# Kernel tuning notes

Hardware: AMD Instinct MI355X
Metric: run time of the kernel (lower is better)

The kernel has to match this reference:

```python
import jax, jax.numpy as jnp
import numpy as np

N_NODES = 100000
IN_CH, HID_CH, OUT_CH = 128, 256, 128
N_EDGES = 1600000
N_LABEL = 200000


def setup_inputs() -> dict:
    key = jax.random.key(0)
    ks = jax.random.split(key, 9)
    x = jax.random.normal(ks[0], (N_NODES, IN_CH), dtype=jnp.float32)
    edge_index = jax.random.randint(ks[1], (2, N_EDGES), 0, N_NODES, dtype=jnp.int64)
    edge_label_index = jax.random.randint(ks[2], (2, N_LABEL), 0, N_NODES, dtype=jnp.int64)
    def glorot(k, fan_in, fan_out):
        s = jnp.sqrt(2.0 / (fan_in + fan_out))
        return jax.random.normal(k, (fan_in, fan_out), dtype=jnp.float32) * s
    # SAGEConv params: lin_l (aggregated neighbors, with bias), lin_r (root, no bias)
    Wl1 = glorot(ks[3], IN_CH, HID_CH)
    bl1 = jnp.zeros((HID_CH,), dtype=jnp.float32)
    Wr1 = glorot(ks[4], IN_CH, HID_CH)
    Wl2 = glorot(ks[5], HID_CH, OUT_CH)
    bl2 = jnp.zeros((OUT_CH,), dtype=jnp.float32)
    Wr2 = glorot(ks[6], HID_CH, OUT_CH)
    return {"x": x, "edge_index": edge_index, "edge_label_index": edge_label_index,
            "Wl1": Wl1, "bl1": bl1, "Wr1": Wr1, "Wl2": Wl2, "bl2": bl2, "Wr2": Wr2}


def _sage_conv(x, src, dst, Wl, bl, Wr):
    # mean aggregation of source-node messages onto destination nodes
    n = x.shape[0]
    agg = jax.ops.segment_sum(x[src], dst, num_segments=n)          # [N, d]
    deg = jax.ops.segment_sum(jnp.ones_like(dst, dtype=x.dtype), dst, num_segments=n)
    agg = agg / jnp.maximum(deg, 1.0)[:, None]
    return agg @ Wl + bl + x @ Wr


def reference(x, edge_index, edge_label_index, Wl1, bl1, Wr1, Wl2, bl2, Wr2):
    src, dst = edge_index[0], edge_index[1]
    h = jax.nn.relu(_sage_conv(x, src, dst, Wl1, bl1, Wr1))
    z = _sage_conv(h, src, dst, Wl2, bl2, Wr2)                      # [N, out]
    lsrc, ldst = edge_label_index[0], edge_label_index[1]
    return jnp.sum(z[lsrc] * z[ldst], axis=-1)                      # [E_label]
```

## Files before the change

kernel.cpp:

```cpp
#include <hip/hip_runtime.h>

#define N_NODES 100000
#define N_EDGES 1600000
#define N_LABEL 200000
#define C_IN 128
#define C_HID 256
#define C_OUT 128

#define BCHUNK 64
#define NBUCK ((N_NODES + BCHUNK - 1) / BCHUNK)
#define NBF 64
#define EPB (N_EDGES / NBF)
#define FLEN (NBUCK * NBF)
#define ESTORE 2048
#define CAST_NB ((N_NODES * C_IN) / (256 * 8))
#define SBLK ((FLEN + 1023) / 1024)

typedef __attribute__((ext_vector_type(8))) short bf16x8;
typedef __attribute__((ext_vector_type(4))) float f32x4;

__device__ __forceinline__ ushort f2bf(float f) {
  uint u = __float_as_uint(f);
  return (ushort)((u + 0x7fffu + ((u >> 16) & 1u)) >> 16);
}

__device__ __forceinline__ uint pack2(float lo, float hi) {
  return (uint)f2bf(lo) | ((uint)f2bf(hi) << 16);
}

__device__ __forceinline__ float bfl(uint u) { return __uint_as_float(u << 16); }
__device__ __forceinline__ float bfh(uint u) {
  return __uint_as_float(u & 0xffff0000u);
}

__device__ __forceinline__ void async_copy16(const void* g, void* lds) {
  __builtin_amdgcn_global_load_lds((const __attribute__((address_space(1))) void*)g,
                                   (__attribute__((address_space(3))) void*)lds,
                                   16, 0, 0);
}

__global__ __launch_bounds__(256) void prep_kernel(const int* __restrict__ dst,
                                                   int* __restrict__ cnt,
                                                   const float* __restrict__ Wl1,
                                                   const float* __restrict__ Wr1,
                                                   const float* __restrict__ Wl2,
                                                   const float* __restrict__ Wr2,
                                                   ushort* __restrict__ WT1,
                                                   ushort* __restrict__ WT2,
                                                   const float* __restrict__ x,
                                                   ushort* __restrict__ xb) {
  __shared__ int lcnt[NBUCK];
  const int blk = blockIdx.x;
  const int t = threadIdx.x;
  if (blk < NBF) {
    const int base = blk * EPB;
    for (int b = t; b < NBUCK; b += 256) lcnt[b] = 0;
    __syncthreads();
    for (int i = t; i < EPB; i += 256) {
      atomicAdd(&lcnt[dst[base + i] >> 6], 1);
    }
    __syncthreads();
    for (int b = t; b < NBUCK; b += 256) cnt[b * NBF + blk] = lcnt[b];
  } else if (blk < NBF + 256) {
    const int n = blk - NBF;
    const int k = t;
    const float v1 = (k < 128) ? Wl1[k * 256 + n] : Wr1[(k - 128) * 256 + n];
    WT1[n * 256 + k] = f2bf(v1);
    const float v2 = (n < 128) ? Wl2[k * 128 + n] : Wr2[k * 128 + (n - 128)];
    WT2[n * 256 + k] = f2bf(v2);
  } else {
    const size_t i = ((size_t)(blk - NBF - 256) * 256 + t) * 8;
    const float4 a = *(const float4*)&x[i];
    const float4 b = *(const float4*)&x[i + 4];
    uint4 o;
    o.x = pack2(a.x, a.y);
    o.y = pack2(a.z, a.w);
    o.z = pack2(b.x, b.y);
    o.w = pack2(b.z, b.w);
    *(uint4*)&xb[i] = o;
  }
}

__global__ __launch_bounds__(256) void scan_sums(const int* __restrict__ a,
                                                 int* __restrict__ bsum) {
  __shared__ int red[256];
  const int t = threadIdx.x;
  const int idx = blockIdx.x * 1024 + t * 4;
  int s = 0;
  if (idx + 3 < FLEN) {
    const int4 v = *(const int4*)&a[idx];
    s = v.x + v.y + v.z + v.w;
  } else {
    for (int j = 0; j < 4 && idx + j < FLEN; ++j) s += a[idx + j];
  }
  red[t] = s;
  __syncthreads();
  for (int off = 128; off > 0; off >>= 1) {
    if (t < off) red[t] += red[t + off];
    __syncthreads();
  }
  if (t == 0) bsum[blockIdx.x] = red[0];
}

__global__ __launch_bounds__(256) void scan_apply(int* __restrict__ a,
                                                  const int* __restrict__ bsum) {
  __shared__ int sh[256];
  __shared__ int bsc[128];
  const int t = threadIdx.x;
  if (t < 128) bsc[t] = (t < SBLK) ? bsum[t] : 0;
  __syncthreads();
  for (int off = 1; off < 128; off <<= 1) {
    int v = 0;
    if (t < 128 && t >= off) v = bsc[t - off];
    __syncthreads();
    if (t < 128 && t >= off) bsc[t] += v;
    __syncthreads();
  }
  const int bbase = (blockIdx.x == 0) ? 0 : bsc[blockIdx.x - 1];
  if (blockIdx.x == SBLK - 1 && t == 0) a[FLEN] = bsc[SBLK - 1];

  const int idx = blockIdx.x * 1024 + t * 4;
  int4 v = make_int4(0, 0, 0, 0);
  const bool full = (idx + 3 < FLEN);
  if (full) {
    v = *(const int4*)&a[idx];
  } else {
    if (idx + 0 < FLEN) v.x = a[idx + 0];
    if (idx + 1 < FLEN) v.y = a[idx + 1];
    if (idx + 2 < FLEN) v.z = a[idx + 2];
    if (idx + 3 < FLEN) v.w = a[idx + 3];
  }
  sh[t] = v.x + v.y + v.z + v.w;
  __syncthreads();
  for (int off = 1; off < 256; off <<= 1) {
    int u = 0;
    if (t >= off) u = sh[t - off];
    __syncthreads();
    if (t >= off) sh[t] += u;
    __syncthreads();
  }
  const int base = bbase + ((t == 0) ? 0 : sh[t - 1]);
  int4 e;
  e.x = base;
  e.y = base + v.x;
  e.z = base + v.x + v.y;
  e.w = base + v.x + v.y + v.z;
  if (full) {
    *(int4*)&a[idx] = e;
  } else {
    if (idx + 0 < FLEN) a[idx + 0] = e.x;
    if (idx + 1 < FLEN) a[idx + 1] = e.y;
    if (idx + 2 < FLEN) a[idx + 2] = e.z;
    if (idx + 3 < FLEN) a[idx + 3] = e.w;
  }
}

__global__ __launch_bounds__(256) void bucket_fill(const int* __restrict__ src,
                                                   const int* __restrict__ dst,
                                                   const int* __restrict__ cnt,
                                                   uint* __restrict__ tmp) {
  __shared__ int lcur[NBUCK];
  const int t = threadIdx.x;
  const int base = blockIdx.x * EPB;
  for (int b = t; b < NBUCK; b += 256) lcur[b] = cnt[b * NBF + blockIdx.x];
  __syncthreads();
  for (int i = t; i < EPB; i += 256) {
    const int d = dst[base + i];
    const int s = src[base + i];
    const int pos = atomicAdd(&lcur[d >> 6], 1);
    tmp[pos] = ((uint)s << 6) | (uint)(d & 63);
  }
}

__global__ __launch_bounds__(256) void csr_build(const int* __restrict__ cnt,
                                                 uint* __restrict__ tmp,
                                                 int* __restrict__ row_start) {
  __shared__ uint est[ESTORE];
  __shared__ uint eso[ESTORE];
  __shared__ int lcnt[BCHUNK];
  __shared__ int lcur[BCHUNK];
  const int b = blockIdx.x;
  const int t = threadIdx.x;
  const int s = cnt[b * NBF];
  const int e = cnt[(b + 1) * NBF];
  const int n = e - s;
  for (int j = t; j < n; j += 256) est[j] = tmp[s + j];
  if (t < BCHUNK) lcnt[t] = 0;
  __syncthreads();
  for (int j = t; j < n; j += 256) atomicAdd(&lcnt[est[j] & 63], 1);
  __syncthreads();
  for (int off = 1; off < BCHUNK; off <<= 1) {
    int v = 0;
    if (t >= off && t < BCHUNK) v = lcnt[t - off];
    __syncthreads();
    if (t >= off && t < BCHUNK) lcnt[t] += v;
    __syncthreads();
  }
  if (t < BCHUNK) {
    const int ex = (t == 0) ? 0 : lcnt[t - 1];
    lcur[t] = ex;
    const int node = b * BCHUNK + t;
    if (node < N_NODES) row_start[node] = s + ex;
  }
  if (b == NBUCK - 1 && t == 0) row_start[N_NODES] = e;
  __syncthreads();
  for (int j = t; j < n; j += 256) {
    const uint v = est[j];
    const int pos = atomicAdd(&lcur[v & 63], 1);
    eso[pos] = v >> 6;
  }
  __syncthreads();
  for (int j = t; j < n; j += 256) tmp[s + j] = eso[j];
}

template <int MODE>
__global__ __launch_bounds__(256) void gather_mean_b(const int* __restrict__ row_start,
                                                     const uint* __restrict__ csr_src,
                                                     const ushort* __restrict__ feat,
                                                     ushort* __restrict__ bout,
                                                     ushort* __restrict__ zb) {
  const int wid = blockIdx.x * 4 + (threadIdx.x >> 6);
  const int lane = threadIdx.x & 63;
  if (wid >= N_NODES) return;
  const int s = row_start[wid];
  const int e = row_start[wid + 1];
  const int slot = lane >> 4;
  const int c0 = (lane & 15) * 8;
  float acc[8] = {};
  int j = s + slot;
#define ACC8(r)                                   \
  acc[0] += bfl(r.x); acc[1] += bfh(r.x);         \
  acc[2] += bfl(r.y); acc[3] += bfh(r.y);         \
  acc[4] += bfl(r.z); acc[5] += bfh(r.z);         \
  acc[6] += bfl(r.w); acc[7] += bfh(r.w);
  for (; j + 12 < e; j += 16) {
    const uint s0 = csr_src[j];
    const uint s1 = csr_src[j + 4];
    const uint s2 = csr_src[j + 8];
    const uint s3 = csr_src[j + 12];
    const uint4 r0 = *(const uint4*)&feat[(size_t)s0 * 128 + c0];
    const uint4 r1 = *(const uint4*)&feat[(size_t)s1 * 128 + c0];
    const uint4 r2 = *(const uint4*)&feat[(size_t)s2 * 128 + c0];
    const uint4 r3 = *(const uint4*)&feat[(size_t)s3 * 128 + c0];
    ACC8(r0) ACC8(r1) ACC8(r2) ACC8(r3)
  }
  for (; j < e; j += 4) {
    const uint s0 = csr_src[j];
    const uint4 r0 = *(const uint4*)&feat[(size_t)s0 * 128 + c0];
    ACC8(r0)
  }
#undef ACC8
#pragma unroll
  for (int k = 0; k < 8; ++k) {
    acc[k] += __shfl_xor(acc[k], 16, 64);
    acc[k] += __shfl_xor(acc[k], 32, 64);
  }
  if (slot == 0) {
    const float rd = 1.0f / fmaxf((float)(e - s), 1.0f);
    if (MODE == 0) {
      uint4 o;
      o.x = pack2(acc[0] * rd, acc[1] * rd);
      o.y = pack2(acc[2] * rd, acc[3] * rd);
      o.z = pack2(acc[4] * rd, acc[5] * rd);
      o.w = pack2(acc[6] * rd, acc[7] * rd);
      *(uint4*)&bout[(size_t)wid * 128 + c0] = o;
    } else {
      uint4 zv = *(const uint4*)&zb[(size_t)wid * 128 + c0];
      uint4 o;
      o.x = pack2(bfl(zv.x) + acc[0] * rd, bfh(zv.x) + acc[1] * rd);
      o.y = pack2(bfl(zv.y) + acc[2] * rd, bfh(zv.y) + acc[3] * rd);
      o.z = pack2(bfl(zv.z) + acc[4] * rd, bfh(zv.z) + acc[5] * rd);
      o.w = pack2(bfl(zv.w) + acc[6] * rd, bfh(zv.w) + acc[7] * rd);
      *(uint4*)&zb[(size_t)wid * 128 + c0] = o;
    }
  }
}

__global__ __launch_bounds__(256) void gemm_fused(const ushort* __restrict__ aggb,
                                                  const ushort* __restrict__ xb,
                                                  const ushort* __restrict__ WT1,
                                                  const ushort* __restrict__ WT2,
                                                  const float* __restrict__ bl1,
                                                  const float* __restrict__ bl2,
                                                  ushort* __restrict__ p,
                                                  ushort* __restrict__ zb) {
  __shared__ ushort As[2048];
  __shared__ ushort Bs[8192];
  __shared__ ushort Ht[64 * 256];
  const int tid = threadIdx.x;
  const int w = tid >> 6;
  const int l = tid & 63;
  const int row0 = blockIdx.x * 64;
  const int wn = w * 64;
  const int fr = l & 15;
  const int kg16 = (l >> 4) * 16;
  const int cr = (l >> 4) * 4;
  const int cc = l & 15;

  const int arow = tid >> 2;
  const int akb = (tid & 3) * 16;
  const int akbs = akb ^ (((arow >> 1) & 3) << 4);
  int agr = row0 + arow;
  agr = (agr < N_NODES) ? agr : (N_NODES - 1);
  const int brow_l = l >> 2;
  const int bkb = (l & 3) * 16;

  {
    f32x4 acc[4][4] = {};
    for (int kc = 0; kc < 8; ++kc) {
      const ushort* Ab = (kc < 4) ? aggb : xb;
      __syncthreads();
      async_copy16((const char*)Ab + (size_t)agr * 256 + (kc & 3) * 64 + akbs,
                   (char*)As + w * 1024);
#pragma unroll
      for (int i_ = 0; i_ < 4; ++i_) {
        const int c_ = w * 4 + i_;
        const int n_ = c_ * 16 + brow_l;
        const int kbs_ = bkb ^ (((n_ >> 1) & 3) << 4);
        async_copy16((const char*)WT1 + (size_t)n_ * 512 + kc * 64 + kbs_,
                     (char*)Bs + c_ * 1024);
      }
      __syncthreads();
      bf16x8 af[4], bfr[4];
#pragma unroll
      for (int i = 0; i < 4; ++i) {
        const int ra = i * 16 + fr;
        const int ba = ra * 64 + (kg16 ^ (((ra >> 1) & 3) << 4));
        af[i] = *(const bf16x8*)((const char*)As + ba);
      }
#pragma unroll
      for (int j = 0; j < 4; ++j) {
        const int nb = wn + j * 16 + fr;
        const int bb = nb * 64 + (kg16 ^ (((nb >> 1) & 3) << 4));
        bfr[j] = *(const bf16x8*)((const char*)Bs + bb);
      }
#pragma unroll
      for (int i = 0; i < 4; ++i)
#pragma unroll
        for (int j = 0; j < 4; ++j)
          acc[i][j] = __builtin_amdgcn_mfma_f32_16x16x32_bf16(af[i], bfr[j],
                                                              acc[i][j], 0, 0, 0);
    }
#pragma unroll
    for (int i = 0; i < 4; ++i) {
#pragma unroll
      for (int j = 0; j < 4; ++j) {
        const int col = wn + j * 16 + cc;
        const float bv = bl1[col];
#pragma unroll
        for (int r = 0; r < 4; ++r) {
          const int row = i * 16 + cr + r;
          const float v = fmaxf(acc[i][j][r] + bv, 0.f);
          const int ba = (row * 512 + col * 2) ^ ((row & 7) << 4);
          *(ushort*)((char*)Ht + ba) = f2bf(v);
        }
      }
    }
  }
  __syncthreads();

  f32x4 acc2[4][4] = {};
#pragma unroll
  for (int kc = 0; kc < 8; ++kc) {
    bf16x8 af[4], bfr[4];
#pragma unroll
    for (int i = 0; i < 4; ++i) {
      const int row = i * 16 + fr;
      const int ba = (row * 512 + kc * 64 + kg16) ^ ((row & 7) << 4);
      af[i] = *(const bf16x8*)((const char*)Ht + ba);
    }
#pragma unroll
    for (int j = 0; j < 4; ++j) {
      const int n = wn + j * 16 + fr;
      bfr[j] = *(const bf16x8*)((const char*)WT2 + (size_t)n * 512 + kc * 64 +
                                kg16);
    }
#pragma unroll
    for (int i = 0; i < 4; ++i)
#pragma unroll
      for (int j = 0; j < 4; ++j)
        acc2[i][j] = __builtin_amdgcn_mfma_f32_16x16x32_bf16(af[i], bfr[j],
                                                             acc2[i][j], 0, 0, 0);
  }
#pragma unroll
  for (int i = 0; i < 4; ++i) {
#pragma unroll
    for (int j = 0; j < 4; ++j) {
      const int col = wn + j * 16 + cc;
      const int gcl = col & 127;
      const bool is_p = (col < 128);
      const float bv = is_p ? 0.f : bl2[gcl];
      ushort* dst = is_p ? p : zb;
#pragma unroll
      for (int r = 0; r < 4; ++r) {
        const int grow = row0 + i * 16 + cr + r;
        if (grow < N_NODES) {
          dst[(size_t)grow * 128 + gcl] = f2bf(acc2[i][j][r] + bv);
        }
      }
    }
  }
}

__global__ __launch_bounds__(256) void dot_kernel(const int* __restrict__ ls,
                                                  const int* __restrict__ ld,
                                                  const ushort* __restrict__ zb,
                                                  float* __restrict__ out) {
  long long tid = (long long)blockIdx.x * 256 + threadIdx.x;
  int e = (int)(tid >> 4);
  int lane = (int)(tid & 15);
  if (e >= N_LABEL) return;
  int a = ls[e], b = ld[e];
  const uint4 va = *(const uint4*)&zb[(size_t)a * 128 + lane * 8];
  const uint4 vb = *(const uint4*)&zb[(size_t)b * 128 + lane * 8];
  float s = bfl(va.x) * bfl(vb.x) + bfh(va.x) * bfh(vb.x) +
            bfl(va.y) * bfl(vb.y) + bfh(va.y) * bfh(vb.y) +
            bfl(va.z) * bfl(vb.z) + bfh(va.z) * bfh(vb.z) +
            bfl(va.w) * bfl(vb.w) + bfh(va.w) * bfh(vb.w);
  s += __shfl_xor(s, 1, 16);
  s += __shfl_xor(s, 2, 16);
  s += __shfl_xor(s, 4, 16);
  s += __shfl_xor(s, 8, 16);
  if (lane == 0) out[e] = s;
}

extern "C" void kernel_launch(void* const* d_in, const int* in_sizes, int n_in,
                              void* d_out, int out_size, void* d_ws, size_t ws_size,
                              hipStream_t stream) {
  const float* x = (const float*)d_in[0];
  const int* ei = (const int*)d_in[1];
  const int* eli = (const int*)d_in[2];
  const float* Wl1 = (const float*)d_in[3];
  const float* bl1 = (const float*)d_in[4];
  const float* Wr1 = (const float*)d_in[5];
  const float* Wl2 = (const float*)d_in[6];
  const float* bl2 = (const float*)d_in[7];
  const float* Wr2 = (const float*)d_in[8];
  float* out = (float*)d_out;

  const int* e_src = ei;
  const int* e_dst = ei + N_EDGES;
  const int* l_src = eli;
  const int* l_dst = eli + N_LABEL;

  char* ws = (char*)d_ws;
  ushort* xb = (ushort*)(ws + 0);
  ushort* aggb = (ushort*)(ws + 25600000);
  ushort* p = (ushort*)(ws + 102400000);
  ushort* zb = (ushort*)(ws + 128000000);
  ushort* WT1 = (ushort*)(ws + 179200000);
  ushort* WT2 = (ushort*)(ws + 179331072);
  uint* tmp = (uint*)(ws + 179462144);
  int* cnt = (int*)(ws + 185862144);
  int* bsum = (int*)(ws + 186270000);
  int* row_start = (int*)(ws + 186280000);

  prep_kernel<<<NBF + 256 + CAST_NB, 256, 0, stream>>>(
      e_dst, cnt, Wl1, Wr1, Wl2, Wr2, WT1, WT2, x, xb);
  scan_sums<<<SBLK, 256, 0, stream>>>(cnt, bsum);
  scan_apply<<<SBLK, 256, 0, stream>>>(cnt, bsum);
  bucket_fill<<<NBF, 256, 0, stream>>>(e_src, e_dst, cnt, tmp);
  csr_build<<<NBUCK, 256, 0, stream>>>(cnt, tmp, row_start);

  gather_mean_b<0><<<(N_NODES + 3) / 4, 256, 0, stream>>>(row_start, tmp, xb,
                                                          aggb, nullptr);
  gemm_fused<<<(N_NODES + 63) / 64, 256, 0, stream>>>(aggb, xb, WT1, WT2, bl1,
                                                      bl2, p, zb);
  gather_mean_b<1><<<(N_NODES + 3) / 4, 256, 0, stream>>>(row_start, tmp, p,
                                                          nullptr, zb);

  dot_kernel<<<(int)(((long long)N_LABEL * 16 + 255) / 256), 256, 0, stream>>>(
      l_src, l_dst, zb, out);
}
```

Baseline: 304.9 us.

## Stage full A tile once in shared memory and read first-layer weights from global

The fused GEMM kernel now loads the whole 64x512 concatenated [agg|x] row tile into one shared buffer up front, replacing the eight per-k-chunk A/B staging rounds and their barriers. First-layer weight fragments are read straight from global or cache, as the second layer already did. The same buffer is reused to hold the ReLU hidden activations after a barrier, which cuts shared memory per block and should allow higher occupancy. The cost is that every wave now issues uncoalesced global weight loads inside the MFMA loop.

```diff
diff --git a/kernel.cpp b/kernel.cpp
--- a/kernel.cpp
+++ b/kernel.cpp
@@ -284,9 +284,7 @@
                                                   const float* __restrict__ bl2,
                                                   ushort* __restrict__ p,
                                                   ushort* __restrict__ zb) {
-  __shared__ ushort As[2048];
-  __shared__ ushort Bs[8192];
-  __shared__ ushort Ht[64 * 256];
+  __shared__ ushort AH[64 * 256];
   const int tid = threadIdx.x;
   const int w = tid >> 6;
   const int l = tid & 63;
@@ -297,77 +295,71 @@
   const int cr = (l >> 4) * 4;
   const int cc = l & 15;
 
-  const int arow = tid >> 2;
-  const int akb = (tid & 3) * 16;
-  const int akbs = akb ^ (((arow >> 1) & 3) << 4);
-  int agr = row0 + arow;
-  agr = (agr < N_NODES) ? agr : (N_NODES - 1);
-  const int brow_l = l >> 2;
-  const int bkb = (l & 3) * 16;
-
-  {
-    f32x4 acc[4][4] = {};
-    for (int kc = 0; kc < 8; ++kc) {
-      const ushort* Ab = (kc < 4) ? aggb : xb;
-      __syncthreads();
-      async_copy16((const char*)Ab + (size_t)agr * 256 + (kc & 3) * 64 + akbs,
-                   (char*)As + w * 1024);
-#pragma unroll
-      for (int i_ = 0; i_ < 4; ++i_) {
-        const int c_ = w * 4 + i_;
-        const int n_ = c_ * 16 + brow_l;
-        const int kbs_ = bkb ^ (((n_ >> 1) & 3) << 4);
-        async_copy16((const char*)WT1 + (size_t)n_ * 512 + kc * 64 + kbs_,
-                     (char*)Bs + c_ * 1024);
-      }
-      __syncthreads();
-      bf16x8 af[4], bfr[4];
-#pragma unroll
-      for (int i = 0; i < 4; ++i) {
-        const int ra = i * 16 + fr;
-        const int ba = ra * 64 + (kg16 ^ (((ra >> 1) & 3) << 4));
-        af[i] = *(const bf16x8*)((const char*)As + ba);
-      }
-#pragma unroll
-      for (int j = 0; j < 4; ++j) {
-        const int nb = wn + j * 16 + fr;
-        const int bb = nb * 64 + (kg16 ^ (((nb >> 1) & 3) << 4));
-        bfr[j] = *(const bf16x8*)((const char*)Bs + bb);
-      }
-#pragma unroll
-      for (int i = 0; i < 4; ++i)
-#pragma unroll
-        for (int j = 0; j < 4; ++j)
-          acc[i][j] = __builtin_amdgcn_mfma_f32_16x16x32_bf16(af[i], bfr[j],
-                                                              acc[i][j], 0, 0, 0);
-    }
-#pragma unroll
-    for (int i = 0; i < 4; ++i) {
-#pragma unroll
-      for (int j = 0; j < 4; ++j) {
-        const int col = wn + j * 16 + cc;
-        const float bv = bl1[col];
-#pragma unroll
-        for (int r = 0; r < 4; ++r) {
-          const int row = i * 16 + cr + r;
-          const float v = fmaxf(acc[i][j][r] + bv, 0.f);
-          const int ba = (row * 512 + col * 2) ^ ((row & 7) << 4);
-          *(ushort*)((char*)Ht + ba) = f2bf(v);
-        }
-      }
-    }
-  }
-  __syncthreads();
-
-  f32x4 acc2[4][4] = {};
+#pragma unroll
+  for (int it = 0; it < 8; ++it) {
+    const int r = it * 8 + w * 2 + (l >> 5);
+    const int cb = (l & 31) * 16;
+    const int cbs = cb ^ ((r & 7) << 4);
+    int node = row0 + r;
+    node = (node < N_NODES) ? node : (N_NODES - 1);
+    const char* src = (cbs < 256)
+        ? (const char*)aggb + (size_t)node * 256 + cbs
+        : (const char*)xb + (size_t)node * 256 + (cbs - 256);
+    async_copy16(src, (char*)AH + it * 4096 + w * 1024);
+  }
+  __syncthreads();
+
+  f32x4 acc[4][4] = {};
 #pragma unroll
   for (int kc = 0; kc < 8; ++kc) {
     bf16x8 af[4], bfr[4];
 #pragma unroll
     for (int i = 0; i < 4; ++i) {
+      const int ra = i * 16 + fr;
+      const int ba = ra * 512 + ((kc * 64 + kg16) ^ ((ra & 7) << 4));
+      af[i] = *(const bf16x8*)((const char*)AH + ba);
+    }
+#pragma unroll
+    for (int j = 0; j < 4; ++j) {
+      const int n = wn + j * 16 + fr;
+      bfr[j] = *(const bf16x8*)((const char*)WT1 + (size_t)n * 512 + kc * 64 +
+                                kg16);
+    }
+#pragma unroll
+    for (int i = 0; i < 4; ++i)
+#pragma unroll
+      for (int j = 0; j < 4; ++j)
+        acc[i][j] = __builtin_amdgcn_mfma_f32_16x16x32_bf16(af[i], bfr[j],
+                                                            acc[i][j], 0, 0, 0);
+  }
+  __syncthreads();
+
+#pragma unroll
+  for (int i = 0; i < 4; ++i) {
+#pragma unroll
+    for (int j = 0; j < 4; ++j) {
+      const int col = wn + j * 16 + cc;
+      const float bv = bl1[col];
+#pragma unroll
+      for (int r = 0; r < 4; ++r) {
+        const int row = i * 16 + cr + r;
+        const float v = fmaxf(acc[i][j][r] + bv, 0.f);
+        const int ba = row * 512 + ((col * 2) ^ ((row & 7) << 4));
+        *(ushort*)((char*)AH + ba) = f2bf(v);
+      }
+    }
+  }
+  __syncthreads();
+
+  f32x4 acc2[4][4] = {};
+#pragma unroll
+  for (int kc = 0; kc < 8; ++kc) {
+    bf16x8 af[4], bfr[4];
+#pragma unroll
+    for (int i = 0; i < 4; ++i) {
       const int row = i * 16 + fr;
-      const int ba = (row * 512 + kc * 64 + kg16) ^ ((row & 7) << 4);
-      af[i] = *(const bf16x8*)((const char*)Ht + ba);
+      const int ba = row * 512 + ((kc * 64 + kg16) ^ ((row & 7) << 4));
+      af[i] = *(const bf16x8*)((const char*)AH + ba);
     }
 #pragma unroll
     for (int j = 0; j < 4; ++j) {
```

Result: slower. 316.2 us (+3.7%).
